# Optimization experiments

Measured on AMD Instinct MI355X. Metric: run time of the kernel, lower is better.

Reference implementation:

```python
import jax, jax.numpy as jnp
import numpy as np
from jax import lax

B, N, D = 4, 2048, 1024
MAX_SEQ = 2048
GROUPS = 4  # math.gcd(1024, 4)
LN_EPS = 1e-5


def setup_inputs() -> dict:
    key = jax.random.key(0)
    ks = jax.random.split(key, 12)
    s = 0.02
    return {
        "x": jax.random.normal(ks[0], (B, N, D), jnp.float32),
        "Wq": jax.random.normal(ks[1], (D, D), jnp.float32) * s,
        "Wk": jax.random.normal(ks[2], (D, D), jnp.float32) * s,
        "Wv": jax.random.normal(ks[3], (D, D), jnp.float32) * s,
        "rel_bias": jax.random.normal(ks[4], (1, MAX_SEQ, MAX_SEQ), jnp.float32) * s,
        "conv_w": jax.random.normal(ks[5], (D, D // GROUPS, 3), jnp.float32) * s,
        "conv_b": jnp.zeros((D,), jnp.float32),
        "resg_w": jax.random.normal(ks[6], (D, D), jnp.float32) * s,
        "resg_b": jnp.zeros((D,), jnp.float32),
        "ln_g": jnp.ones((D,), jnp.float32),
        "ln_b": jnp.zeros((D,), jnp.float32),
        "fc1_w": jax.random.normal(ks[7], (D // 2, D), jnp.float32) * s,
        "fc1_b": jnp.zeros((D // 2,), jnp.float32),
        "fc2_w": jax.random.normal(ks[8], (1, D // 2), jnp.float32) * s,
        "fc2_b": jnp.zeros((1,), jnp.float32),
    }


def _forward(x, Wq, Wk, Wv, rel_bias, conv_w, conv_b, resg_w, resg_b,
             ln_g, ln_b, fc1_w, fc1_b, fc2_w, fc2_b):
    b, n, d = x.shape
    scale = 1.0 / jnp.sqrt(jnp.asarray(d, x.dtype))
    q = x @ Wq.T  # [b,n,dk]
    k = x @ Wk.T
    v = x @ Wv.T  # [b,n,dv]
    att = jnp.einsum("bqd,bkd->bqk", q, k) * scale + rel_bias[:, :n, :n]
    causal = jnp.tril(jnp.ones((n, n), bool))
    att = jnp.where(causal, att, jnp.asarray(-jnp.inf, att.dtype))
    att = jax.nn.softmax(att, axis=-1)  # dropout is identity at eval
    att_out = jnp.einsum("bqk,bkd->bqd", att, v)
    # grouped temporal conv over sequence dim: v [b,n,dv] -> NCH [b,dv,n]
    conv = lax.conv_general_dilated(
        v.transpose(0, 2, 1), conv_w, window_strides=(1,), padding=[(1, 1)],
        dimension_numbers=("NCH", "OIH", "NCH"), feature_group_count=GROUPS)
    conv = conv + conv_b[None, :, None]
    out = att_out + conv.transpose(0, 2, 1)
    res = jax.nn.sigmoid(out @ resg_w.T + resg_b)
    out = x + res * out
    mu = out.mean(-1, keepdims=True)
    var = out.var(-1, keepdims=True)
    out = (out - mu) * lax.rsqrt(var + LN_EPS) * ln_g + ln_b
    h = jax.nn.gelu(out @ fc1_w.T + fc1_b, approximate=False)
    return jax.nn.sigmoid(h @ fc2_w.T + fc2_b)


def reference(x, Wq, Wk, Wv, rel_bias, conv_w, conv_b, resg_w, resg_b,
              ln_g, ln_b, fc1_w, fc1_b, fc2_w, fc2_b):
    return _forward(x, Wq, Wk, Wv, rel_bias, conv_w, conv_b, resg_w, resg_b,
                    ln_g, ln_b, fc1_w, fc1_b, fc2_w, fc2_b)
```

## Files before the change

### kernel.cpp

```cpp
#include <hip/hip_runtime.h>
#include <math.h>

#define NSEQ 2048
#define DDIM 1024
#define BSZ  4
#define BM 128
#define BN 128
#define BK 32

typedef short bf16x8 __attribute__((ext_vector_type(8)));
typedef float f32x4 __attribute__((ext_vector_type(4)));
typedef unsigned int u32;
typedef unsigned short u16;

__device__ __forceinline__ u16 f2bf(float f) {
  union { float f; u32 u; } x; x.f = f;
  u32 r = x.u + 0x7FFFu + ((x.u >> 16) & 1u);
  return (u16)(r >> 16);
}
__device__ __forceinline__ float bf2f(u16 h) {
  union { u32 u; float f; } x; x.u = ((u32)h) << 16; return x.f;
}
__device__ __forceinline__ float sigmoidf_(float x) {
  return 1.0f / (1.0f + expf(-x));
}

__device__ __forceinline__ void async_copy16(const u16* g, u16* l) {
  __builtin_amdgcn_global_load_lds(
      (const __attribute__((address_space(1))) u32*)g,
      (__attribute__((address_space(3))) u32*)l, 16, 0, 0);
}

__device__ __forceinline__ void stage_tile(const u16* __restrict__ gsrc, size_t ld,
                                           int k0, u16* lds, int tid) {
  const int wave = tid >> 6, lane = tid & 63;
  const int rr = lane >> 2;
  const int kg = (lane & 3) ^ ((lane >> 3) & 3);
  const int cc = kg << 3;
#pragma unroll
  for (int j = 0; j < 2; ++j) {
    const int c = j * 4 + wave;
    async_copy16(gsrc + (size_t)(c * 16 + rr) * ld + k0 + cc, lds + c * 512);
  }
}

__device__ __forceinline__ void mfma_step(const u16* Al, const u16* Bl,
                                          int wr, int wc, int l16, int quad,
                                          f32x4 acc[4][4]) {
  const int qs = (quad ^ ((l16 >> 1) & 3)) << 3;
  bf16x8 a[4], b[4];
#pragma unroll
  for (int i = 0; i < 4; ++i) {
    a[i] = *(const bf16x8*)(Al + (wr * 64 + i * 16 + l16) * BK + qs);
    b[i] = *(const bf16x8*)(Bl + (wc * 64 + i * 16 + l16) * BK + qs);
  }
#pragma unroll
  for (int i = 0; i < 4; ++i)
#pragma unroll
    for (int j = 0; j < 4; ++j)
      acc[i][j] = __builtin_amdgcn_mfma_f32_16x16x32_bf16(a[i], b[j], acc[i][j], 0, 0, 0);
}

__device__ __forceinline__ void zero_acc(f32x4 acc[4][4]) {
#pragma unroll
  for (int i = 0; i < 4; ++i)
#pragma unroll
    for (int j = 0; j < 4; ++j) {
      f32x4 z = {0.f, 0.f, 0.f, 0.f};
      acc[i][j] = z;
    }
}

__device__ __forceinline__ void gemm_loop(const u16* A, size_t lda,
                                          const u16* Bt, size_t ldb, int K,
                                          u16* Al, u16* Bl, int tid,
                                          int wr, int wc, int l16, int quad,
                                          f32x4 acc[4][4]) {
  for (int k0 = 0; k0 < K; k0 += BK) {
    __syncthreads();
    stage_tile(A, lda, k0, Al, tid);
    stage_tile(Bt, ldb, k0, Bl, tid);
    __syncthreads();
    mfma_step(Al, Bl, wr, wc, l16, quad, acc);
  }
}

__global__ __launch_bounds__(256) void k_prep(
    const float* __restrict__ x,  const float* __restrict__ Wq,
    const float* __restrict__ Wk, const float* __restrict__ Wv,
    const float* __restrict__ rw, const float* __restrict__ f1w,
    const float* __restrict__ cw,
    u16* __restrict__ xb,  u16* __restrict__ Wqb, u16* __restrict__ Wkb,
    u16* __restrict__ Wvb, u16* __restrict__ rwb, u16* __restrict__ f1wb,
    u16* __restrict__ cwp, u16* __restrict__ vpad)
{
  const int blk = blockIdx.x, tid = threadIdx.x;
  const float* s; u16* d; int base;
  if (blk < 8192)       { s = x;   d = xb;   base = blk; }
  else if (blk < 9216)  { s = Wq;  d = Wqb;  base = blk - 8192; }
  else if (blk < 10240) { s = Wk;  d = Wkb;  base = blk - 9216; }
  else if (blk < 11264) { s = Wv;  d = Wvb;  base = blk - 10240; }
  else if (blk < 12288) { s = rw;  d = rwb;  base = blk - 11264; }
  else if (blk < 12800) { s = f1w; d = f1wb; base = blk - 12288; }
  else if (blk < 13824) {
    const int o = blk - 12800, i = tid;
#pragma unroll
    for (int tap = 0; tap < 3; ++tap)
      cwp[(size_t)o * 768 + tap * 256 + i] = f2bf(cw[(size_t)o * 768 + i * 3 + tap]);
    return;
  } else {
    const int e = blk - 13824, bb = e >> 1, which = e & 1;
    u16* row = vpad + (size_t)bb * 2050 * 1024 + (which ? (size_t)2049 * 1024 : 0);
    ushort4 z = {0, 0, 0, 0};
    ((ushort4*)row)[tid] = z;
    return;
  }
  const int i = base * 256 + tid;
  const float4 v = ((const float4*)s)[i];
  ushort4 o;
  o.x = f2bf(v.x); o.y = f2bf(v.y); o.z = f2bf(v.z); o.w = f2bf(v.w);
  ((ushort4*)d)[i] = o;
}

__global__ __launch_bounds__(256) void k_qkv(
    const u16* __restrict__ xb, const u16* __restrict__ Wqb,
    const u16* __restrict__ Wkb, const u16* __restrict__ Wvb,
    u16* __restrict__ qb, u16* __restrict__ kb, u16* __restrict__ vpad)
{
  __shared__ u16 Al[BM * BK], Bl[BN * BK];
  const int tid = threadIdx.x, z = blockIdx.z;
  const u16* W = (z == 0) ? Wqb : ((z == 1) ? Wkb : Wvb);
  const int row0 = blockIdx.x * BM, col0 = blockIdx.y * BN;
  const int lane = tid & 63, wave = tid >> 6;
  const int quad = lane >> 4, l16 = lane & 15, wr = wave >> 1, wc = wave & 1;
  f32x4 acc[4][4];
  zero_acc(acc);
  gemm_loop(xb + (size_t)row0 * DDIM, DDIM, W + (size_t)col0 * DDIM, DDIM, DDIM,
            Al, Bl, tid, wr, wc, l16, quad, acc);
#pragma unroll
  for (int mi = 0; mi < 4; ++mi)
#pragma unroll
    for (int r = 0; r < 4; ++r) {
      const int grow = row0 + wr * 64 + mi * 16 + quad * 4 + r;
#pragma unroll
      for (int ni = 0; ni < 4; ++ni) {
        const int gcol = col0 + wc * 64 + ni * 16 + l16;
        const u16 hv = f2bf(acc[mi][ni][r]);
        if (z == 2) {
          const int b = grow >> 11, t = grow & 2047;
          vpad[(size_t)b * 2050 * 1024 + 1024 + (size_t)t * 1024 + gcol] = hv;
        } else {
          (z == 0 ? qb : kb)[(size_t)grow * DDIM + gcol] = hv;
        }
      }
    }
}

__global__ __launch_bounds__(256) void k_vt(const u16* __restrict__ vpad,
                                            u16* __restrict__ vT)
{
  __shared__ u16 tile[64][72];
  const int t0 = blockIdx.x * 64, d0 = blockIdx.y * 64, b = blockIdx.z;
  const int tid = threadIdx.x;
  const u16* vb = vpad + (size_t)b * 2050 * 1024 + 1024;
#pragma unroll
  for (int p = 0; p < 4; ++p) {
    const int r = p * 16 + (tid >> 4), c = (tid & 15) << 2;
    const ushort4 v4 = *(const ushort4*)(vb + (size_t)(t0 + r) * 1024 + d0 + c);
    tile[r][c] = v4.x; tile[r][c + 1] = v4.y; tile[r][c + 2] = v4.z; tile[r][c + 3] = v4.w;
  }
  __syncthreads();
  u16* ob = vT + (size_t)b * DDIM * NSEQ;
#pragma unroll
  for (int p = 0; p < 4; ++p) {
    const int d = p * 16 + (tid >> 4), t = (tid & 15) << 2;
    ushort4 o;
    o.x = tile[t][d]; o.y = tile[t + 1][d]; o.z = tile[t + 2][d]; o.w = tile[t + 3][d];
    *(ushort4*)(ob + (size_t)(d0 + d) * NSEQ + t0 + t) = o;
  }
}

__global__ __launch_bounds__(256) void k_scores(
    const u16* __restrict__ qb, const u16* __restrict__ kb,
    const float* __restrict__ rb, float* __restrict__ att)
{
  const int it = blockIdx.x, jt = blockIdx.y, b = blockIdx.z;
  if (jt > it) return;
  __shared__ u16 Al[BM * BK], Bl[BN * BK];
  const int tid = threadIdx.x;
  const int row0 = it * BM, col0 = jt * BN;
  const int lane = tid & 63, wave = tid >> 6;
  const int quad = lane >> 4, l16 = lane & 15, wr = wave >> 1, wc = wave & 1;
  f32x4 acc[4][4];
  zero_acc(acc);
  gemm_loop(qb + ((size_t)b * NSEQ + row0) * DDIM, DDIM,
            kb + ((size_t)b * NSEQ + col0) * DDIM, DDIM, DDIM,
            Al, Bl, tid, wr, wc, l16, quad, acc);
  float* abase = att + (size_t)b * NSEQ * NSEQ;
#pragma unroll
  for (int mi = 0; mi < 4; ++mi)
#pragma unroll
    for (int r = 0; r < 4; ++r) {
      const int i = row0 + wr * 64 + mi * 16 + quad * 4 + r;
#pragma unroll
      for (int ni = 0; ni < 4; ++ni) {
        const int j = col0 + wc * 64 + ni * 16 + l16;
        abase[(size_t)i * NSEQ + j] =
            acc[mi][ni][r] * 0.03125f + rb[(size_t)i * NSEQ + j];
      }
    }
}

__global__ __launch_bounds__(256) void k_softmax(const float* __restrict__ att,
                                                 u16* __restrict__ attb)
{
  const int i = blockIdx.x, b = blockIdx.y;
  const float* row = att + ((size_t)b * NSEQ + i) * NSEQ;
  u16* orow = attb + ((size_t)b * NSEQ + i) * NSEQ;
  const int valid = i + 1;
  const int wlen = ((i >> 7) + 1) << 7;
  const int tid = threadIdx.x;
  const int lane = tid & 63, wid = tid >> 6;

  float v[8];
  float m = -1e30f;
#pragma unroll
  for (int t = 0; t < 8; ++t) {
    const int idx = tid + (t << 8);
    v[t] = (idx < valid) ? row[idx] : -1e30f;
    m = fmaxf(m, v[t]);
  }
#pragma unroll
  for (int off = 32; off; off >>= 1) m = fmaxf(m, __shfl_xor(m, off));
  __shared__ float red[4];
  if (lane == 0) red[wid] = m;
  __syncthreads();
  m = fmaxf(fmaxf(red[0], red[1]), fmaxf(red[2], red[3]));
  __syncthreads();

  float s = 0.f;
#pragma unroll
  for (int t = 0; t < 8; ++t) {
    const int idx = tid + (t << 8);
    float e = (idx < valid) ? expf(v[t] - m) : 0.f;
    v[t] = e;
    s += e;
  }
#pragma unroll
  for (int off = 32; off; off >>= 1) s += __shfl_xor(s, off);
  if (lane == 0) red[wid] = s;
  __syncthreads();
  s = red[0] + red[1] + red[2] + red[3];
  const float inv = 1.0f / s;
#pragma unroll
  for (int t = 0; t < 8; ++t) {
    const int idx = tid + (t << 8);
    if (idx < wlen) orow[idx] = f2bf(v[t] * inv);
  }
}

__global__ __launch_bounds__(256) void k_pv(
    const u16* __restrict__ attb, const u16* __restrict__ vT,
    float* __restrict__ buf1)
{
  __shared__ u16 Al[BM * BK], Bl[BN * BK];
  const int it = blockIdx.x, nt = blockIdx.y, b = blockIdx.z;
  const int tid = threadIdx.x;
  const int row0 = it * BM, col0 = nt * BN;
  const int K = (it + 1) * BM;
  const int lane = tid & 63, wave = tid >> 6;
  const int quad = lane >> 4, l16 = lane & 15, wr = wave >> 1, wc = wave & 1;
  f32x4 acc[4][4];
  zero_acc(acc);
  gemm_loop(attb + ((size_t)b * NSEQ + row0) * NSEQ, NSEQ,
            vT + ((size_t)b * DDIM + col0) * NSEQ, NSEQ, K,
            Al, Bl, tid, wr, wc, l16, quad, acc);
  float* obase = buf1 + (size_t)b * NSEQ * DDIM;
#pragma unroll
  for (int mi = 0; mi < 4; ++mi)
#pragma unroll
    for (int r = 0; r < 4; ++r) {
      const int grow = row0 + wr * 64 + mi * 16 + quad * 4 + r;
#pragma unroll
      for (int ni = 0; ni < 4; ++ni) {
        const int gcol = col0 + wc * 64 + ni * 16 + l16;
        obase[(size_t)grow * DDIM + gcol] = acc[mi][ni][r];
      }
    }
}

__global__ __launch_bounds__(256) void k_conv(
    const u16* __restrict__ vpad, const u16* __restrict__ cwp,
    const float* __restrict__ cb, float* __restrict__ buf1,
    u16* __restrict__ buf1b)
{
  __shared__ u16 Al[BM * BK], Bl[BN * BK];
  const int tid = threadIdx.x;
  const int row0 = blockIdx.x * BM;
  const int col0 = blockIdx.y * BN;
  const int g = col0 >> 8;
  const int b = row0 >> 11, t0 = row0 & 2047;
  const u16* vb = vpad + (size_t)b * 2050 * 1024 + 1024;
  const u16* Bbase = cwp + (size_t)col0 * 768;
  const int lane = tid & 63, wave = tid >> 6;
  const int quad = lane >> 4, l16 = lane & 15, wr = wave >> 1, wc = wave & 1;
  const int rr = lane >> 2;
  const int kg = (lane & 3) ^ ((lane >> 3) & 3);
  const int cc = kg << 3;
  const int gch = g << 8;
  f32x4 acc[4][4];
  zero_acc(acc);
  for (int k0 = 0; k0 < 768; k0 += BK) {
    __syncthreads();
    const int tap = k0 >> 8;
    const int i0 = k0 & 255;
#pragma unroll
    for (int j = 0; j < 2; ++j) {
      const int c = j * 4 + wave;
      const int r = c * 16 + rr;
      async_copy16(vb + (size_t)(t0 + r - 1 + tap) * 1024 + gch + i0 + cc,
                   Al + c * 512);
    }
    stage_tile(Bbase, 768, k0, Bl, tid);
    __syncthreads();
    mfma_step(Al, Bl, wr, wc, l16, quad, acc);
  }
#pragma unroll
  for (int mi = 0; mi < 4; ++mi)
#pragma unroll
    for (int r = 0; r < 4; ++r) {
      const int grow = row0 + wr * 64 + mi * 16 + quad * 4 + r;
#pragma unroll
      for (int ni = 0; ni < 4; ++ni) {
        const int gcol = col0 + wc * 64 + ni * 16 + l16;
        const size_t idx = (size_t)grow * DDIM + gcol;
        const float val = buf1[idx] + cb[gcol] + acc[mi][ni][r];
        buf1[idx] = val;
        buf1b[idx] = f2bf(val);
      }
    }
}

__global__ __launch_bounds__(256) void k_resgate(
    const u16* __restrict__ buf1b, const u16* __restrict__ rwb,
    const float* __restrict__ rbias, const float* __restrict__ x,
    const float* __restrict__ buf1, float* __restrict__ buf2)
{
  __shared__ u16 Al[BM * BK], Bl[BN * BK];
  const int tid = threadIdx.x;
  const int row0 = blockIdx.x * BM, col0 = blockIdx.y * BN;
  const int lane = tid & 63, wave = tid >> 6;
  const int quad = lane >> 4, l16 = lane & 15, wr = wave >> 1, wc = wave & 1;
  f32x4 acc[4][4];
  zero_acc(acc);
  gemm_loop(buf1b + (size_t)row0 * DDIM, DDIM, rwb + (size_t)col0 * DDIM, DDIM,
            DDIM, Al, Bl, tid, wr, wc, l16, quad, acc);
#pragma unroll
  for (int mi = 0; mi < 4; ++mi)
#pragma unroll
    for (int r = 0; r < 4; ++r) {
      const int grow = row0 + wr * 64 + mi * 16 + quad * 4 + r;
#pragma unroll
      for (int ni = 0; ni < 4; ++ni) {
        const int gcol = col0 + wc * 64 + ni * 16 + l16;
        const size_t idx = (size_t)grow * DDIM + gcol;
        const float gate = sigmoidf_(acc[mi][ni][r] + rbias[gcol]);
        buf2[idx] = x[idx] + gate * buf1[idx];
      }
    }
}

__global__ __launch_bounds__(256) void k_ln(
    const float* __restrict__ buf, const float* __restrict__ gw,
    const float* __restrict__ gb, u16* __restrict__ outb)
{
  const int row = blockIdx.x;
  const float* p = buf + (size_t)row * DDIM;
  const int tid = threadIdx.x;
  const int lane = tid & 63, wid = tid >> 6;
  const int c = tid << 2;
  float4 val = *(const float4*)(p + c);
  float s = val.x + val.y + val.z + val.w;
  float s2 = val.x * val.x + val.y * val.y + val.z * val.z + val.w * val.w;
#pragma unroll
  for (int off = 32; off; off >>= 1) {
    s += __shfl_xor(s, off);
    s2 += __shfl_xor(s2, off);
  }
  __shared__ float r1[4], r2[4];
  if (lane == 0) { r1[wid] = s; r2[wid] = s2; }
  __syncthreads();
  s = r1[0] + r1[1] + r1[2] + r1[3];
  s2 = r2[0] + r2[1] + r2[2] + r2[3];
  const float mean = s * (1.0f / DDIM);
  const float var = s2 * (1.0f / DDIM) - mean * mean;
  const float rstd = rsqrtf(var + 1e-5f);
  const float4 g4 = *(const float4*)(gw + c);
  const float4 b4 = *(const float4*)(gb + c);
  ushort4 o;
  o.x = f2bf((val.x - mean) * rstd * g4.x + b4.x);
  o.y = f2bf((val.y - mean) * rstd * g4.y + b4.y);
  o.z = f2bf((val.z - mean) * rstd * g4.z + b4.z);
  o.w = f2bf((val.w - mean) * rstd * g4.w + b4.w);
  *(ushort4*)(outb + (size_t)row * DDIM + c) = o;
}

__global__ __launch_bounds__(256) void k_fc1(
    const u16* __restrict__ A, const u16* __restrict__ W,
    const float* __restrict__ bias, float* __restrict__ h)
{
  __shared__ u16 Al[BM * BK], Bl[BN * BK];
  const int tid = threadIdx.x;
  const int row0 = blockIdx.x * BM, col0 = blockIdx.y * BN;
  const int lane = tid & 63, wave = tid >> 6;
  const int quad = lane >> 4, l16 = lane & 15, wr = wave >> 1, wc = wave & 1;
  f32x4 acc[4][4];
  zero_acc(acc);
  gemm_loop(A + (size_t)row0 * DDIM, DDIM, W + (size_t)col0 * DDIM, DDIM, DDIM,
            Al, Bl, tid, wr, wc, l16, quad, acc);
#pragma unroll
  for (int mi = 0; mi < 4; ++mi)
#pragma unroll
    for (int r = 0; r < 4; ++r) {
      const int grow = row0 + wr * 64 + mi * 16 + quad * 4 + r;
#pragma unroll
      for (int ni = 0; ni < 4; ++ni) {
        const int gcol = col0 + wc * 64 + ni * 16 + l16;
        const float t = acc[mi][ni][r] + bias[gcol];
        h[(size_t)grow * 512 + gcol] = 0.5f * t * (1.0f + erff(t * 0.70710678118654752f));
      }
    }
}

__global__ __launch_bounds__(256) void k_fc2(
    const float* __restrict__ h, const float* __restrict__ w,
    const float* __restrict__ b2, float* __restrict__ out)
{
  const int r = blockIdx.x * 4 + (threadIdx.x >> 6);
  const int lane = threadIdx.x & 63;
  const float* hp = h + (size_t)r * 512;
  float s = 0.f;
#pragma unroll
  for (int t = 0; t < 8; ++t) {
    const int c = lane + t * 64;
    s = fmaf(hp[c], w[c], s);
  }
#pragma unroll
  for (int off = 32; off; off >>= 1) s += __shfl_xor(s, off);
  if (lane == 0) out[r] = sigmoidf_(s + b2[0]);
}

extern "C" void kernel_launch(void* const* d_in, const int* in_sizes, int n_in,
                              void* d_out, int out_size, void* d_ws, size_t ws_size,
                              hipStream_t stream) {
  const float* x    = (const float*)d_in[0];
  const float* Wq   = (const float*)d_in[1];
  const float* Wk   = (const float*)d_in[2];
  const float* Wv   = (const float*)d_in[3];
  const float* rb   = (const float*)d_in[4];
  const float* cw   = (const float*)d_in[5];
  const float* cb   = (const float*)d_in[6];
  const float* rw   = (const float*)d_in[7];
  const float* rbias= (const float*)d_in[8];
  const float* lng  = (const float*)d_in[9];
  const float* lnb  = (const float*)d_in[10];
  const float* f1w  = (const float*)d_in[11];
  const float* f1b  = (const float*)d_in[12];
  const float* f2w  = (const float*)d_in[13];
  const float* f2b  = (const float*)d_in[14];
  float* out = (float*)d_out;
  char* w8 = (char*)d_ws;

  u16* xb    = (u16*)(w8 + 0);
  u16* Wqb   = (u16*)(w8 + 16777216);
  u16* Wkb   = (u16*)(w8 + 18874368);
  u16* Wvb   = (u16*)(w8 + 20971520);
  u16* rwb   = (u16*)(w8 + 23068672);
  u16* f1wb  = (u16*)(w8 + 25165824);
  u16* cwp   = (u16*)(w8 + 26214400);
  u16* qb    = (u16*)(w8 + 27787264);
  u16* kb    = (u16*)(w8 + 44564480);
  u16* vpad  = (u16*)(w8 + 61341696);
  u16* vT    = (u16*)(w8 + 78135296);
  float* att = (float*)(w8 + 94912512);
  u16*   attb  = (u16*)(w8 + 27787264);
  float* buf1  = (float*)(w8 + 94912512);
  u16*   buf1b = (u16*)(w8 + 0);
  float* buf2  = (float*)(w8 + 128466944);
  u16*   ln16  = (u16*)(w8 + 78135296);
  float* h     = (float*)(w8 + 61341696);

  k_prep   <<<dim3(13832),     256, 0, stream>>>(x, Wq, Wk, Wv, rw, f1w, cw,
                                                 xb, Wqb, Wkb, Wvb, rwb, f1wb,
                                                 cwp, vpad);
  k_qkv    <<<dim3(64, 8, 3),  256, 0, stream>>>(xb, Wqb, Wkb, Wvb, qb, kb, vpad);
  k_vt     <<<dim3(32, 16, 4), 256, 0, stream>>>(vpad, vT);
  k_scores <<<dim3(16, 16, 4), 256, 0, stream>>>(qb, kb, rb, att);
  k_softmax<<<dim3(NSEQ, BSZ), 256, 0, stream>>>(att, attb);
  k_pv     <<<dim3(16, 8, 4),  256, 0, stream>>>(attb, vT, buf1);
  k_conv   <<<dim3(64, 8),     256, 0, stream>>>(vpad, cwp, cb, buf1, buf1b);
  k_resgate<<<dim3(64, 8),     256, 0, stream>>>(buf1b, rwb, rbias, x, buf1, buf2);
  k_ln     <<<dim3(BSZ * NSEQ),256, 0, stream>>>(buf2, lng, lnb, ln16);
  k_fc1    <<<dim3(64, 4),     256, 0, stream>>>(ln16, f1wb, f1b, h);
  k_fc2    <<<dim3(NSEQ),      256, 0, stream>>>(h, f2w, f2b, out);
}
```

Baseline: 415.8 us.

## Double GEMM K-tile to 64 and store intermediates in bf16

Raises the shared GEMM K-step from 32 to 64, with a new XOR swizzle and two MFMA sub-steps per tile, so there are half as many barrier/staging iterations. Separately, the PV output, the conv+attention sum, the residual-gated buffer and the fc1 activations are now stored as bf16 instead of fp32, which cuts global memory traffic in the epilogues and in the LayerNorm and fc2 kernels. The cost is extra rounding on the residual path before LayerNorm and a larger LDS footprint per block.

```diff
diff --git a/kernel.cpp b/kernel.cpp
--- a/kernel.cpp
+++ b/kernel.cpp
@@ -6,7 +6,7 @@
 #define BSZ  4
 #define BM 128
 #define BN 128
-#define BK 32
+#define BK 64
 
 typedef short bf16x8 __attribute__((ext_vector_type(8)));
 typedef float f32x4 __attribute__((ext_vector_type(4)));
@@ -34,31 +34,34 @@
 __device__ __forceinline__ void stage_tile(const u16* __restrict__ gsrc, size_t ld,
                                            int k0, u16* lds, int tid) {
   const int wave = tid >> 6, lane = tid & 63;
-  const int rr = lane >> 2;
-  const int kg = (lane & 3) ^ ((lane >> 3) & 3);
-  const int cc = kg << 3;
-#pragma unroll
-  for (int j = 0; j < 2; ++j) {
+  const int rr = lane >> 3;
+  const int q  = (lane & 7) ^ rr;
+#pragma unroll
+  for (int j = 0; j < 4; ++j) {
     const int c = j * 4 + wave;
-    async_copy16(gsrc + (size_t)(c * 16 + rr) * ld + k0 + cc, lds + c * 512);
+    async_copy16(gsrc + (size_t)(c * 8 + rr) * ld + k0 + q * 8, lds + c * 512);
   }
 }
 
 __device__ __forceinline__ void mfma_step(const u16* Al, const u16* Bl,
                                           int wr, int wc, int l16, int quad,
                                           f32x4 acc[4][4]) {
-  const int qs = (quad ^ ((l16 >> 1) & 3)) << 3;
-  bf16x8 a[4], b[4];
-#pragma unroll
-  for (int i = 0; i < 4; ++i) {
-    a[i] = *(const bf16x8*)(Al + (wr * 64 + i * 16 + l16) * BK + qs);
-    b[i] = *(const bf16x8*)(Bl + (wc * 64 + i * 16 + l16) * BK + qs);
-  }
-#pragma unroll
-  for (int i = 0; i < 4; ++i)
-#pragma unroll
-    for (int j = 0; j < 4; ++j)
-      acc[i][j] = __builtin_amdgcn_mfma_f32_16x16x32_bf16(a[i], b[j], acc[i][j], 0, 0, 0);
+  const int r7 = l16 & 7;
+#pragma unroll
+  for (int ks = 0; ks < 2; ++ks) {
+    const int s = ((ks * 4 + quad) ^ r7) << 3;
+    bf16x8 a[4], b[4];
+#pragma unroll
+    for (int i = 0; i < 4; ++i) {
+      a[i] = *(const bf16x8*)(Al + (wr * 64 + i * 16 + l16) * BK + s);
+      b[i] = *(const bf16x8*)(Bl + (wc * 64 + i * 16 + l16) * BK + s);
+    }
+#pragma unroll
+    for (int i = 0; i < 4; ++i)
+#pragma unroll
+      for (int j = 0; j < 4; ++j)
+        acc[i][j] = __builtin_amdgcn_mfma_f32_16x16x32_bf16(a[i], b[j], acc[i][j], 0, 0, 0);
+  }
 }
 
 __device__ __forceinline__ void zero_acc(f32x4 acc[4][4]) {
@@ -261,7 +264,7 @@
 
 __global__ __launch_bounds__(256) void k_pv(
     const u16* __restrict__ attb, const u16* __restrict__ vT,
-    float* __restrict__ buf1)
+    u16* __restrict__ pvb)
 {
   __shared__ u16 Al[BM * BK], Bl[BN * BK];
   const int it = blockIdx.x, nt = blockIdx.y, b = blockIdx.z;
@@ -275,7 +278,7 @@
   gemm_loop(attb + ((size_t)b * NSEQ + row0) * NSEQ, NSEQ,
             vT + ((size_t)b * DDIM + col0) * NSEQ, NSEQ, K,
             Al, Bl, tid, wr, wc, l16, quad, acc);
-  float* obase = buf1 + (size_t)b * NSEQ * DDIM;
+  u16* obase = pvb + (size_t)b * NSEQ * DDIM;
 #pragma unroll
   for (int mi = 0; mi < 4; ++mi)
 #pragma unroll
@@ -284,14 +287,14 @@
 #pragma unroll
       for (int ni = 0; ni < 4; ++ni) {
         const int gcol = col0 + wc * 64 + ni * 16 + l16;
-        obase[(size_t)grow * DDIM + gcol] = acc[mi][ni][r];
+        obase[(size_t)grow * DDIM + gcol] = f2bf(acc[mi][ni][r]);
       }
     }
 }
 
 __global__ __launch_bounds__(256) void k_conv(
     const u16* __restrict__ vpad, const u16* __restrict__ cwp,
-    const float* __restrict__ cb, float* __restrict__ buf1,
+    const float* __restrict__ cb, const u16* __restrict__ pvb,
     u16* __restrict__ buf1b)
 {
   __shared__ u16 Al[BM * BK], Bl[BN * BK];
@@ -304,9 +307,8 @@
   const u16* Bbase = cwp + (size_t)col0 * 768;
   const int lane = tid & 63, wave = tid >> 6;
   const int quad = lane >> 4, l16 = lane & 15, wr = wave >> 1, wc = wave & 1;
-  const int rr = lane >> 2;
-  const int kg = (lane & 3) ^ ((lane >> 3) & 3);
-  const int cc = kg << 3;
+  const int rr = lane >> 3;
+  const int q  = (lane & 7) ^ rr;
   const int gch = g << 8;
   f32x4 acc[4][4];
   zero_acc(acc);
@@ -315,10 +317,10 @@
     const int tap = k0 >> 8;
     const int i0 = k0 & 255;
 #pragma unroll
-    for (int j = 0; j < 2; ++j) {
+    for (int j = 0; j < 4; ++j) {
       const int c = j * 4 + wave;
-      const int r = c * 16 + rr;
-      async_copy16(vb + (size_t)(t0 + r - 1 + tap) * 1024 + gch + i0 + cc,
+      const int r = c * 8 + rr;
+      async_copy16(vb + (size_t)(t0 + r - 1 + tap) * 1024 + gch + i0 + q * 8,
                    Al + c * 512);
     }
     stage_tile(Bbase, 768, k0, Bl, tid);
@@ -334,9 +336,7 @@
       for (int ni = 0; ni < 4; ++ni) {
         const int gcol = col0 + wc * 64 + ni * 16 + l16;
         const size_t idx = (size_t)grow * DDIM + gcol;
-        const float val = buf1[idx] + cb[gcol] + acc[mi][ni][r];
-        buf1[idx] = val;
-        buf1b[idx] = f2bf(val);
+        buf1b[idx] = f2bf(bf2f(pvb[idx]) + cb[gcol] + acc[mi][ni][r]);
       }
     }
 }
@@ -344,7 +344,7 @@
 __global__ __launch_bounds__(256) void k_resgate(
     const u16* __restrict__ buf1b, const u16* __restrict__ rwb,
     const float* __restrict__ rbias, const float* __restrict__ x,
-    const float* __restrict__ buf1, float* __restrict__ buf2)
+    u16* __restrict__ buf2)
 {
   __shared__ u16 Al[BM * BK], Bl[BN * BK];
   const int tid = threadIdx.x;
@@ -365,21 +365,23 @@
         const int gcol = col0 + wc * 64 + ni * 16 + l16;
         const size_t idx = (size_t)grow * DDIM + gcol;
         const float gate = sigmoidf_(acc[mi][ni][r] + rbias[gcol]);
-        buf2[idx] = x[idx] + gate * buf1[idx];
+        buf2[idx] = f2bf(x[idx] + gate * bf2f(buf1b[idx]));
       }
     }
 }
 
 __global__ __launch_bounds__(256) void k_ln(
-    const float* __restrict__ buf, const float* __restrict__ gw,
+    const u16* __restrict__ buf, const float* __restrict__ gw,
     const float* __restrict__ gb, u16* __restrict__ outb)
 {
   const int row = blockIdx.x;
-  const float* p = buf + (size_t)row * DDIM;
+  const u16* p = buf + (size_t)row * DDIM;
   const int tid = threadIdx.x;
   const int lane = tid & 63, wid = tid >> 6;
   const int c = tid << 2;
-  float4 val = *(const float4*)(p + c);
+  const ushort4 raw = *(const ushort4*)(p + c);
+  float4 val;
+  val.x = bf2f(raw.x); val.y = bf2f(raw.y); val.z = bf2f(raw.z); val.w = bf2f(raw.w);
   float s = val.x + val.y + val.z + val.w;
   float s2 = val.x * val.x + val.y * val.y + val.z * val.z + val.w * val.w;
 #pragma unroll
@@ -407,7 +409,7 @@
 
 __global__ __launch_bounds__(256) void k_fc1(
     const u16* __restrict__ A, const u16* __restrict__ W,
-    const float* __restrict__ bias, float* __restrict__ h)
+    const float* __restrict__ bias, u16* __restrict__ h)
 {
   __shared__ u16 Al[BM * BK], Bl[BN * BK];
   const int tid = threadIdx.x;
@@ -427,23 +429,24 @@
       for (int ni = 0; ni < 4; ++ni) {
         const int gcol = col0 + wc * 64 + ni * 16 + l16;
         const float t = acc[mi][ni][r] + bias[gcol];
-        h[(size_t)grow * 512 + gcol] = 0.5f * t * (1.0f + erff(t * 0.70710678118654752f));
+        h[(size_t)grow * 512 + gcol] =
+            f2bf(0.5f * t * (1.0f + erff(t * 0.70710678118654752f)));
       }
     }
 }
 
 __global__ __launch_bounds__(256) void k_fc2(
-    const float* __restrict__ h, const float* __restrict__ w,
+    const u16* __restrict__ h, const float* __restrict__ w,
     const float* __restrict__ b2, float* __restrict__ out)
 {
   const int r = blockIdx.x * 4 + (threadIdx.x >> 6);
   const int lane = threadIdx.x & 63;
-  const float* hp = h + (size_t)r * 512;
+  const u16* hp = h + (size_t)r * 512;
   float s = 0.f;
 #pragma unroll
   for (int t = 0; t < 8; ++t) {
     const int c = lane + t * 64;
-    s = fmaf(hp[c], w[c], s);
+    s = fmaf(bf2f(hp[c]), w[c], s);
   }
 #pragma unroll
   for (int off = 32; off; off >>= 1) s += __shfl_xor(s, off);
@@ -483,12 +486,12 @@
   u16* vpad  = (u16*)(w8 + 61341696);
   u16* vT    = (u16*)(w8 + 78135296);
   float* att = (float*)(w8 + 94912512);
-  u16*   attb  = (u16*)(w8 + 27787264);
-  float* buf1  = (float*)(w8 + 94912512);
-  u16*   buf1b = (u16*)(w8 + 0);
-  float* buf2  = (float*)(w8 + 128466944);
-  u16*   ln16  = (u16*)(w8 + 78135296);
-  float* h     = (float*)(w8 + 61341696);
+  u16* attb  = (u16*)(w8 + 27787264);
+  u16* pvb   = (u16*)(w8 + 94912512);
+  u16* buf1b = (u16*)(w8 + 27787264);
+  u16* buf2  = (u16*)(w8 + 111689728);
+  u16* ln16  = (u16*)(w8 + 78135296);
+  u16* h     = (u16*)(w8 + 61341696);
 
   k_prep   <<<dim3(13832),     256, 0, stream>>>(x, Wq, Wk, Wv, rw, f1w, cw,
                                                  xb, Wqb, Wkb, Wvb, rwb, f1wb,
@@ -497,9 +500,9 @@
   k_vt     <<<dim3(32, 16, 4), 256, 0, stream>>>(vpad, vT);
   k_scores <<<dim3(16, 16, 4), 256, 0, stream>>>(qb, kb, rb, att);
   k_softmax<<<dim3(NSEQ, BSZ), 256, 0, stream>>>(att, attb);
-  k_pv     <<<dim3(16, 8, 4),  256, 0, stream>>>(attb, vT, buf1);
-  k_conv   <<<dim3(64, 8),     256, 0, stream>>>(vpad, cwp, cb, buf1, buf1b);
-  k_resgate<<<dim3(64, 8),     256, 0, stream>>>(buf1b, rwb, rbias, x, buf1, buf2);
+  k_pv     <<<dim3(16, 8, 4),  256, 0, stream>>>(attb, vT, pvb);
+  k_conv   <<<dim3(64, 8),     256, 0, stream>>>(vpad, cwp, cb, pvb, buf1b);
+  k_resgate<<<dim3(64, 8),     256, 0, stream>>>(buf1b, rwb, rbias, x, buf2);
   k_ln     <<<dim3(BSZ * NSEQ),256, 0, stream>>>(buf2, lng, lnb, ln16);
   k_fc1    <<<dim3(64, 4),     256, 0, stream>>>(ln16, f1wb, f1b, h);
   k_fc2    <<<dim3(NSEQ),      256, 0, stream>>>(h, f2w, f2b, out);
```

New measurement: 383.8 us. -7.7%, faster.
